# Performance work log

Measured on AMD Instinct MI355X. Metric: run time of the kernel, lower is better.

## Reference

```python
import jax, jax.numpy as jnp
import numpy as np

DIM = 2048
H = 16        # num query heads
HK = 2        # num kv heads
D = DIM // H  # head_dim = 128
G = H // HK   # q heads per kv head = 8
SCALE = 1.0 / np.sqrt(D)


def setup_inputs() -> dict:
    key = jax.random.key(0)
    ks = jax.random.split(key, 9)
    xavier = lambda k, fi, fo: jax.random.uniform(k, (fi, fo), jnp.float32,
                                                  -np.sqrt(6.0 / (fi + fo)), np.sqrt(6.0 / (fi + fo)))
    return {
        "x": jax.random.normal(ks[0], (2, 2048, DIM), jnp.float32),
        "Wq": xavier(ks[1], DIM, H * D),  "bq": jnp.zeros((H * D,), jnp.float32),
        "Wk": xavier(ks[2], DIM, HK * D), "bk": jnp.zeros((HK * D,), jnp.float32),
        "Wv": xavier(ks[3], DIM, HK * D), "bv": jnp.zeros((HK * D,), jnp.float32),
        "Wo": xavier(ks[4], H * D, DIM),  "bo": jnp.zeros((DIM,), jnp.float32),
    }


def reference(x, Wq, bq, Wk, bk, Wv, bv, Wo, bo):
    B, T, C = x.shape
    # projections; q grouped as (kv_head, group) so repeat_interleave becomes a broadcast
    q = (x @ Wq + bq).reshape(B, T, HK, G, D)   # [B,T,Hk,G,D]
    k = (x @ Wk + bk).reshape(B, T, HK, D)      # [B,T,Hk,D]
    v = (x @ Wv + bv).reshape(B, T, HK, D)
    # scores: [B,Hk,G,Tq,Tk] — shared K broadcast across the G query heads per kv head
    scores = jnp.einsum('bqhgd,bshd->bhgqs', q, k) * SCALE
    scores = jnp.clip(scores, -100.0, 100.0)
    attn = jax.nn.softmax(scores, axis=-1)
    out = jnp.einsum('bhgqs,bshd->bqhgd', attn, v).reshape(B, T, H * D)
    return out @ Wo + bo
```

## Files before the change

kernel.cpp:

```cpp
#include <hip/hip_runtime.h>
#include <cstdint>

typedef __bf16 bf16x8 __attribute__((ext_vector_type(8)));
typedef float floatx4 __attribute__((ext_vector_type(4)));
typedef float floatx16 __attribute__((ext_vector_type(16)));
typedef unsigned short u16;
typedef unsigned int u32;

#define SCALE2 0.1275434297677098f
#define CLIP2  144.26950408889634f
#define DEFER  8.0f

__device__ __forceinline__ u16 f2bf(float f) {
  union { float f; u32 i; } v; v.f = f;
  u32 r = v.i + 0x7fffu + ((v.i >> 16) & 1u);
  return (u16)(r >> 16);
}

__device__ __forceinline__ u32 cvtpk(float lo, float hi) {
  u32 r;
  asm("v_cvt_pk_bf16_f32 %0, %1, %2" : "=v"(r) : "v"(lo), "v"(hi));
  return r;
}

__device__ __forceinline__ void gll16(const void* g, void* l) {
  __builtin_amdgcn_global_load_lds(
      (const __attribute__((address_space(1))) u32*)g,
      (__attribute__((address_space(3))) u32*)l, 16, 0, 0);
}

__global__ __launch_bounds__(256) void convert_bf16(
    const float* __restrict__ src, u16* __restrict__ dst, int n4) {
  int i = blockIdx.x * 256 + threadIdx.x;
  if (i >= n4) return;
  float4 v = ((const float4*)src)[i];
  ushort4 o;
  o.x = f2bf(v.x); o.y = f2bf(v.y); o.z = f2bf(v.z); o.w = f2bf(v.w);
  ((ushort4*)dst)[i] = o;
}

__global__ __launch_bounds__(256) void transpose_cat(
    const float* __restrict__ W0, const float* __restrict__ W1,
    const float* __restrict__ W2,
    int n1, int n2, int ld0, int ld1, int ld2, int K, u16* __restrict__ Bt) {
  __shared__ u16 tile[32][33];
  const int k0 = blockIdx.x * 32, n0 = blockIdx.y * 32;
  const float* src; int ld, nb;
  if (n0 < n1)      { src = W0; ld = ld0; nb = n0; }
  else if (n0 < n2) { src = W1; ld = ld1; nb = n0 - n1; }
  else              { src = W2; ld = ld2; nb = n0 - n2; }
  const int tx = threadIdx.x, ty = threadIdx.y;
#pragma unroll
  for (int i = 0; i < 4; i++) {
    int k = ty + i * 8;
    tile[k][tx] = f2bf(src[(size_t)(k0 + k) * ld + nb + tx]);
  }
  __syncthreads();
#pragma unroll
  for (int i = 0; i < 4; i++) {
    int n = ty + i * 8;
    Bt[(size_t)(n0 + n) * K + k0 + tx] = tile[tx][n];
  }
}

template <int EPI>
__global__ __launch_bounds__(256) void gemm_bt(
    const u16* __restrict__ A, const u16* __restrict__ Bt,
    const float* __restrict__ bias0, const float* __restrict__ bias1,
    const float* __restrict__ bias2,
    u16* __restrict__ out0, u16* __restrict__ out1, u16* __restrict__ out2,
    float* __restrict__ outf,
    int M, int N, int K) {
  __shared__ u16 As[2][128][32];
  __shared__ u16 Bs[2][128][32];
  const int tid  = threadIdx.x;
  const int w    = tid >> 6, L = tid & 63, ln = L & 15, quad = L >> 4;
  const int m0   = blockIdx.y * 128, n0 = blockIdx.x * 128;
  const int mw   = (w & 1) * 64, nw = (w >> 1) * 64;
  const int sr = w * 32 + (L >> 2), sc = (L & 3) * 8;
  const u16* ga = &A [(size_t)(m0 + sr) * K + sc];
  const u16* gb = &Bt[(size_t)(n0 + sr) * K + sc];
  floatx4 acc[4][4] = {};
  const int nk = K >> 5;

  gll16(ga, &As[0][w * 32][0]);
  gll16(ga + (size_t)16 * K, &As[0][w * 32 + 16][0]);
  gll16(gb, &Bs[0][w * 32][0]);
  gll16(gb + (size_t)16 * K, &Bs[0][w * 32 + 16][0]);

  for (int i = 0; i < nk; i++) {
    const int cur = i & 1;
    __syncthreads();
    if (i + 1 < nk) {
      const int kt = (i + 1) << 5;
      gll16(ga + kt, &As[cur ^ 1][w * 32][0]);
      gll16(ga + (size_t)16 * K + kt, &As[cur ^ 1][w * 32 + 16][0]);
      gll16(gb + kt, &Bs[cur ^ 1][w * 32][0]);
      gll16(gb + (size_t)16 * K + kt, &Bs[cur ^ 1][w * 32 + 16][0]);
    }
    bf16x8 af[4], bf[4];
#pragma unroll
    for (int mb = 0; mb < 4; mb++) af[mb] = *(const bf16x8*)&As[cur][mw + mb * 16 + ln][quad * 8];
#pragma unroll
    for (int nb = 0; nb < 4; nb++) bf[nb] = *(const bf16x8*)&Bs[cur][nw + nb * 16 + ln][quad * 8];
#pragma unroll
    for (int mb = 0; mb < 4; mb++)
#pragma unroll
      for (int nb = 0; nb < 4; nb++)
        acc[mb][nb] = __builtin_amdgcn_mfma_f32_16x16x32_bf16(af[mb], bf[nb], acc[mb][nb], 0, 0, 0);
  }

#pragma unroll
  for (int mb = 0; mb < 4; mb++) {
#pragma unroll
    for (int nb = 0; nb < 4; nb++) {
#pragma unroll
      for (int r = 0; r < 4; r++) {
        const int m = m0 + mw + mb * 16 + quad * 4 + r;
        const int n = n0 + nw + nb * 16 + ln;
        float v = acc[mb][nb][r];
        if constexpr (EPI == 0) {
          if (n < 2048) {
            v = (v + bias0[n]) * SCALE2;
            out0[(size_t)m * 2048 + n] = f2bf(v);
          } else if (n < 2304) {
            const int j = n - 2048;
            v += bias1[j];
            out1[(size_t)m * 256 + j] = f2bf(v);
          } else {
            const int j = n - 2304;
            v += bias2[j];
            const int b = m >> 11, t = m & 2047;
            out2[((size_t)(b * 256 + j)) * 2048 + t] = f2bf(v);
          }
        } else {
          v += bias0[n];
          outf[(size_t)m * (size_t)N + n] = v;
        }
      }
    }
  }
}

__global__ __launch_bounds__(256, 2) void attn_kernel(
    const u16* __restrict__ Q, const u16* __restrict__ K,
    const u16* __restrict__ Vt, u16* __restrict__ O) {
  __shared__ u16 Ksh[2][16 * 512];
  __shared__ u16 Vsh[2][16 * 512];
  const int tid = threadIdx.x;
  const int w = tid >> 6, L = tid & 63;
  const int ln = L & 31, hf = L >> 5;
  const int qt = blockIdx.x, h = blockIdx.y, b = blockIdx.z;
  const int hk = h >> 3;
  const size_t qrow0 = (size_t)b * 2048 + qt * 128 + w * 32;

  const u16* Kbase = K + (size_t)b * 2048 * 256 + hk * 128;
  const u16* Vbase = Vt + (size_t)(b * 2 + hk) * 128 * 2048;

  const u16* gK[4];
  const u16* gV[4];
#pragma unroll
  for (int j = 0; j < 4; j++) {
    const int fK = 4 * w + j, mb = fK >> 3, kc = fK & 7;
    gK[j] = Kbase + (size_t)(mb * 32 + ln) * 256 + kc * 16 + hf * 8;
    const int fV = 4 * w + j, db = fV >> 2, ks = fV & 3;
    gV[j] = Vbase + (size_t)(db * 32 + ln) * 2048 + ks * 16 + hf * 8;
  }

  bf16x8 qf[8];
#pragma unroll
  for (int kc = 0; kc < 8; kc++)
    qf[kc] = *(const bf16x8*)&Q[(qrow0 + ln) * 2048 + h * 128 + kc * 16 + hf * 8];

  floatx16 oT[4] = {};
  float mrow = -1e30f, lrow = 0.f;

#pragma unroll
  for (int j = 0; j < 4; j++) {
    gll16(gK[j], &Ksh[0][(4 * w + j) * 512]);
    gll16(gV[j], &Vsh[0][(4 * w + j) * 512]);
  }

  for (int i = 0; i < 32; i++) {
    const int cur = i & 1;
    __syncthreads();
    if (i < 31) {
#pragma unroll
      for (int j = 0; j < 4; j++) {
        gll16(gK[j] + (size_t)(i + 1) * 64 * 256, &Ksh[cur ^ 1][(4 * w + j) * 512]);
        gll16(gV[j] + (size_t)(i + 1) * 64, &Vsh[cur ^ 1][(4 * w + j) * 512]);
      }
    }

    floatx16 sf[2] = {};
#pragma unroll
    for (int kc = 0; kc < 8; kc++) {
#pragma unroll
      for (int mb = 0; mb < 2; mb++) {
        bf16x8 kf = *(const bf16x8*)&Ksh[cur][(mb * 8 + kc) * 512 + L * 8];
        sf[mb] = __builtin_amdgcn_mfma_f32_32x32x16_bf16(kf, qf[kc], sf[mb], 0, 0, 0);
      }
    }

    float mx = -1e30f;
#pragma unroll
    for (int mb = 0; mb < 2; mb++)
#pragma unroll
      for (int r = 0; r < 16; r++) {
        sf[mb][r] = __builtin_amdgcn_fmed3f(sf[mb][r], -CLIP2, CLIP2);
        mx = fmaxf(mx, sf[mb][r]);
      }
    mx = fmaxf(mx, __shfl_xor(mx, 32));

    const bool need = __ballot(mx > mrow + DEFER) != 0;
    float mn = mrow;
    float alpha = 1.f;
    if (need) {
      mn = fmaxf(mrow, mx);
      alpha = __builtin_amdgcn_exp2f(mrow - mn);
      mrow = mn;
    }

    float s = 0.f;
#pragma unroll
    for (int mb = 0; mb < 2; mb++)
#pragma unroll
      for (int r = 0; r < 16; r++) {
        const float p = __builtin_amdgcn_exp2f(sf[mb][r] - mn);
        sf[mb][r] = p;
        s += p;
      }
    s += __shfl_xor(s, 32);
    if (need) {
      lrow = lrow * alpha + s;
#pragma unroll
      for (int db = 0; db < 4; db++)
#pragma unroll
        for (int r = 0; r < 16; r++) oT[db][r] *= alpha;
    } else {
      lrow += s;
    }

#pragma unroll
    for (int ks = 0; ks < 4; ks++) {
      const int mb = ks >> 1, s8 = (ks & 1) * 8;
      u32 cA0 = cvtpk(sf[mb][s8 + 0], sf[mb][s8 + 1]);
      u32 cA1 = cvtpk(sf[mb][s8 + 2], sf[mb][s8 + 3]);
      u32 cB0 = cvtpk(sf[mb][s8 + 4], sf[mb][s8 + 5]);
      u32 cB1 = cvtpk(sf[mb][s8 + 6], sf[mb][s8 + 7]);
      asm("v_permlane32_swap_b32 %0, %1" : "+v"(cA0), "+v"(cB0));
      asm("v_permlane32_swap_b32 %0, %1" : "+v"(cA1), "+v"(cB1));
      union { u32 u[4]; bf16x8 v; } pb;
      pb.u[0] = cA0; pb.u[1] = cA1; pb.u[2] = cB0; pb.u[3] = cB1;
#pragma unroll
      for (int db = 0; db < 4; db++) {
        bf16x8 vf = *(const bf16x8*)&Vsh[cur][(db * 4 + ks) * 512 + L * 8];
        oT[db] = __builtin_amdgcn_mfma_f32_32x32x16_bf16(vf, pb.v, oT[db], 0, 0, 0);
      }
    }
  }

  const float inv = 1.f / lrow;
  u16* orow = O + (qrow0 + ln) * 2048 + h * 128;
#pragma unroll
  for (int db = 0; db < 4; db++) {
#pragma unroll
    for (int g = 0; g < 4; g++) {
      uint2 st;
      st.x = cvtpk(oT[db][g * 4 + 0] * inv, oT[db][g * 4 + 1] * inv);
      st.y = cvtpk(oT[db][g * 4 + 2] * inv, oT[db][g * 4 + 3] * inv);
      *(uint2*)&orow[db * 32 + g * 8 + hf * 4] = st;
    }
  }
}

extern "C" void kernel_launch(void* const* d_in, const int* in_sizes, int n_in,
                              void* d_out, int out_size, void* d_ws, size_t ws_size,
                              hipStream_t stream) {
  const float* x  = (const float*)d_in[0];
  const float* Wq = (const float*)d_in[1];
  const float* bq = (const float*)d_in[2];
  const float* Wk = (const float*)d_in[3];
  const float* bk = (const float*)d_in[4];
  const float* Wv = (const float*)d_in[5];
  const float* bv = (const float*)d_in[6];
  const float* Wo = (const float*)d_in[7];
  const float* bo = (const float*)d_in[8];
  float* out = (float*)d_out;

  char* ws = (char*)d_ws;
  u16* xb     = (u16*)(ws);
  u16* Ob     = (u16*)(ws);
  u16* Wqkv_t = (u16*)(ws + 16777216);
  u16* Wot    = (u16*)(ws + 27262976);
  u16* Qb     = (u16*)(ws + 35651584);
  u16* Kb     = (u16*)(ws + 52428800);
  u16* Vtb    = (u16*)(ws + 54525952);
  (void)in_sizes; (void)n_in; (void)out_size; (void)ws_size;

  convert_bf16<<<8192, 256, 0, stream>>>(x, xb, 2097152);

  transpose_cat<<<dim3(64, 80), dim3(32, 8), 0, stream>>>(
      Wq, Wk, Wv, 2048, 2304, 2048, 256, 256, 2048, Wqkv_t);
  transpose_cat<<<dim3(64, 64), dim3(32, 8), 0, stream>>>(
      Wo, Wo, Wo, 2048, 2048, 2048, 2048, 2048, 2048, Wot);

  gemm_bt<0><<<dim3(20, 32), 256, 0, stream>>>(
      xb, Wqkv_t, bq, bk, bv, Qb, Kb, Vtb, nullptr, 4096, 2560, 2048);

  attn_kernel<<<dim3(16, 16, 2), 256, 0, stream>>>(Qb, Kb, Vtb, Ob);

  gemm_bt<1><<<dim3(16, 32), 256, 0, stream>>>(
      Ob, Wot, bo, nullptr, nullptr, nullptr, nullptr, nullptr, out, 4096, 2048, 2048);
}
```

Before: 337.3 us.

## Software-pipeline flash attention: overlap next QK^T with current PV and softmax

Restructures the attention main loop into a two-stage ping-pong pipeline. The QK^T MFMAs for the next KV tile are issued alongside the PV MFMAs of the current tile, with s_setprio raising wave priority around the MFMA bursts. The row max and row sum reductions become tree reductions instead of serial chains, to shorten dependency latency. In exchange it holds two score register sets, which raises register pressure, and adds extra barriers per tile.

After: 328.5 us. 2.6% less time.

```diff
diff --git a/kernel.cpp b/kernel.cpp
--- a/kernel.cpp
+++ b/kernel.cpp
@@ -175,62 +175,61 @@
   floatx16 oT[4] = {};
   float mrow = -1e30f, lrow = 0.f;
 
-#pragma unroll
-  for (int j = 0; j < 4; j++) {
-    gll16(gK[j], &Ksh[0][(4 * w + j) * 512]);
-    gll16(gV[j], &Vsh[0][(4 * w + j) * 512]);
-  }
-
-  for (int i = 0; i < 32; i++) {
-    const int cur = i & 1;
-    __syncthreads();
-    if (i < 31) {
-#pragma unroll
-      for (int j = 0; j < 4; j++) {
-        gll16(gK[j] + (size_t)(i + 1) * 64 * 256, &Ksh[cur ^ 1][(4 * w + j) * 512]);
-        gll16(gV[j] + (size_t)(i + 1) * 64, &Vsh[cur ^ 1][(4 * w + j) * 512]);
-      }
-    }
-
-    floatx16 sf[2] = {};
+  auto issue = [&](int tile, int bufi) {
+#pragma unroll
+    for (int j = 0; j < 4; j++) {
+      gll16(gK[j] + (size_t)tile * 64 * 256, &Ksh[bufi][(4 * w + j) * 512]);
+      gll16(gV[j] + (size_t)tile * 64,       &Vsh[bufi][(4 * w + j) * 512]);
+    }
+  };
+
+  auto qkt = [&](floatx16 (&sf)[2], const u16* kb) {
+#pragma unroll
+    for (int r = 0; r < 16; r++) { sf[0][r] = 0.f; sf[1][r] = 0.f; }
 #pragma unroll
     for (int kc = 0; kc < 8; kc++) {
 #pragma unroll
       for (int mb = 0; mb < 2; mb++) {
-        bf16x8 kf = *(const bf16x8*)&Ksh[cur][(mb * 8 + kc) * 512 + L * 8];
+        bf16x8 kf = *(const bf16x8*)&kb[(mb * 8 + kc) * 512 + L * 8];
         sf[mb] = __builtin_amdgcn_mfma_f32_32x32x16_bf16(kf, qf[kc], sf[mb], 0, 0, 0);
       }
     }
-
-    float mx = -1e30f;
+  };
+
+  auto softmax = [&](floatx16 (&sf)[2]) {
 #pragma unroll
     for (int mb = 0; mb < 2; mb++)
 #pragma unroll
-      for (int r = 0; r < 16; r++) {
+      for (int r = 0; r < 16; r++)
         sf[mb][r] = __builtin_amdgcn_fmed3f(sf[mb][r], -CLIP2, CLIP2);
-        mx = fmaxf(mx, sf[mb][r]);
-      }
-    mx = fmaxf(mx, __shfl_xor(mx, 32));
-
+    float t16[16];
+#pragma unroll
+    for (int r = 0; r < 16; r++) t16[r] = fmaxf(sf[0][r], sf[1][r]);
+#pragma unroll
+    for (int d = 8; d >= 1; d >>= 1)
+#pragma unroll
+      for (int r = 0; r < d; r++) t16[r] = fmaxf(t16[r], t16[r + d]);
+    const float mx = fmaxf(t16[0], __shfl_xor(t16[0], 32));
     const bool need = __ballot(mx > mrow + DEFER) != 0;
-    float mn = mrow;
-    float alpha = 1.f;
+    float mn = mrow, alpha = 1.f;
     if (need) {
       mn = fmaxf(mrow, mx);
       alpha = __builtin_amdgcn_exp2f(mrow - mn);
       mrow = mn;
     }
-
-    float s = 0.f;
 #pragma unroll
     for (int mb = 0; mb < 2; mb++)
 #pragma unroll
-      for (int r = 0; r < 16; r++) {
-        const float p = __builtin_amdgcn_exp2f(sf[mb][r] - mn);
-        sf[mb][r] = p;
-        s += p;
-      }
-    s += __shfl_xor(s, 32);
+      for (int r = 0; r < 16; r++)
+        sf[mb][r] = __builtin_amdgcn_exp2f(sf[mb][r] - mn);
+    float s16[16];
+#pragma unroll
+    for (int r = 0; r < 16; r++) s16[r] = sf[0][r] + sf[1][r];
+#pragma unroll
+    for (int d = 8; d >= 1; d >>= 1)
+#pragma unroll
+      for (int r = 0; r < d; r++) s16[r] += s16[r + d];
+    const float s = s16[0] + __shfl_xor(s16[0], 32);
     if (need) {
       lrow = lrow * alpha + s;
 #pragma unroll
@@ -240,7 +239,9 @@
     } else {
       lrow += s;
     }
-
+  };
+
+  auto pv = [&](floatx16 (&sf)[2], const u16* vb) {
 #pragma unroll
     for (int ks = 0; ks < 4; ks++) {
       const int mb = ks >> 1, s8 = (ks & 1) * 8;
@@ -254,10 +255,36 @@
       pb.u[0] = cA0; pb.u[1] = cA1; pb.u[2] = cB0; pb.u[3] = cB1;
 #pragma unroll
       for (int db = 0; db < 4; db++) {
-        bf16x8 vf = *(const bf16x8*)&Vsh[cur][(db * 4 + ks) * 512 + L * 8];
+        bf16x8 vf = *(const bf16x8*)&vb[(db * 4 + ks) * 512 + L * 8];
         oT[db] = __builtin_amdgcn_mfma_f32_32x32x16_bf16(vf, pb.v, oT[db], 0, 0, 0);
       }
     }
+  };
+
+  floatx16 sfA[2], sfB[2];
+
+  issue(0, 0);
+  __syncthreads();
+  issue(1, 1);
+  qkt(sfA, &Ksh[0][0]);
+
+  for (int t = 0; t < 32; t += 2) {
+    softmax(sfA);
+    __syncthreads();
+    __builtin_amdgcn_s_setprio(1);
+    qkt(sfB, &Ksh[1][0]);
+    pv(sfA, &Vsh[0][0]);
+    __builtin_amdgcn_s_setprio(0);
+    __syncthreads();
+    if (t + 2 < 32) issue(t + 2, 0);
+    softmax(sfB);
+    __syncthreads();
+    __builtin_amdgcn_s_setprio(1);
+    if (t + 2 < 32) qkt(sfA, &Ksh[0][0]);
+    pv(sfB, &Vsh[1][0]);
+    __builtin_amdgcn_s_setprio(0);
+    __syncthreads();
+    if (t + 3 < 32) issue(t + 3, 1);
   }
 
   const float inv = 1.f / lrow;
```
